# Kernel optimization log

Hardware: AMD Instinct MI355X
Metric: run time of the kernel (lower is better)

Reference implementation:

```python
import jax, jax.numpy as jnp
import numpy as np

B, N, M, H = 32, 1024, 256, 128


def setup_inputs() -> dict:
    key = jax.random.key(0)
    kA, kh, kW1, kW2 = jax.random.split(key, 4)
    A = jax.random.uniform(kA, (B, N, N), dtype=jnp.float32)
    h = jax.random.normal(kh, (B, N, M), dtype=jnp.float32)
    # torch Linear default init scale ~ 1/sqrt(fan_in)
    W1 = jax.random.normal(kW1, (M, H), dtype=jnp.float32) / np.sqrt(M)
    b1 = jnp.zeros((H,), dtype=jnp.float32)
    W2 = jax.random.normal(kW2, (H, M), dtype=jnp.float32) / np.sqrt(H)
    b2 = jnp.zeros((M,), dtype=jnp.float32)
    return {"A": A, "h": h, "W1": W1, "b1": b1, "W2": W2, "b2": b2}


def reference(A, h, W1, b1, W2, b2):
    # k = bmm(A, h) / 3 : [B,N,M]
    k = jnp.einsum('bij,bjm->bim', A, h) / 3.0
    # eta_g: Linear -> ReLU -> Linear
    k = jax.nn.relu(k @ W1 + b1) @ W2 + b2
    # A_mask = max over last dim of A, keepdims -> [B,N,1]
    A_mask = jnp.max(A, axis=-1, keepdims=True)
    # gated combine: k*mask + h*(mask-1)*(-1) == k*mask + h*(1-mask)
    return k * A_mask + h * (1.0 - A_mask)
```

## Files before the change

kernel.cpp:

```cpp
#include <hip/hip_runtime.h>

typedef __attribute__((ext_vector_type(8))) short bf16x8;
typedef __attribute__((ext_vector_type(4))) float f32x4;
typedef __attribute__((ext_vector_type(8))) unsigned short u16x8;

#define BB 32
#define NN 1024
#define MM 256
#define HH 128

__device__ __forceinline__ unsigned short f2bf(float f) {
  union { float f; unsigned int u; } c; c.f = f;
  unsigned int u = c.u + 0x7fffu + ((c.u >> 16) & 1u);
  return (unsigned short)(u >> 16);
}
__device__ __forceinline__ unsigned int cvtpk(float lo, float hi) {
  unsigned int r;
  asm("v_cvt_pk_bf16_f32 %0, %1, %2" : "=v"(r) : "v"(lo), "v"(hi));
  return r;
}
__device__ __forceinline__ float4 gload_f4(const float* p) {
  float4 r;
  asm volatile("global_load_dwordx4 %0, %1, off" : "=v"(r) : "v"(p));
  return r;
}
typedef __attribute__((address_space(3))) unsigned int as3_u32;
typedef const __attribute__((address_space(1))) unsigned int as1_u32;
__device__ __forceinline__ void gl_lds16(const void* g, void* l) {
  __builtin_amdgcn_global_load_lds((as1_u32*)g, (as3_u32*)l, 16, 0, 0);
}

__global__ __launch_bounds__(256)
void k_prep(const float* __restrict__ hg, unsigned short* __restrict__ hTg,
            const float* __restrict__ W1, const float* __restrict__ W2,
            unsigned short* __restrict__ W1T, unsigned short* __restrict__ W2T) {
  int bid = blockIdx.x;
  if (bid < BB * 64) {
    __shared__ unsigned short tile[64][65];
    int b = bid >> 6;
    int t = bid & 63;
    int k0 = (t >> 2) << 6;
    int m0 = (t & 3) << 6;
    int tt = threadIdx.x;
    {
      int r = tt >> 2;
      int cg = (tt & 3) << 4;
      const float* src = hg + (((size_t)b * NN + k0 + r) * MM + m0 + cg);
#pragma unroll
      for (int i = 0; i < 4; ++i) {
        float4 v = reinterpret_cast<const float4*>(src)[i];
        tile[r][cg + i * 4 + 0] = f2bf(v.x);
        tile[r][cg + i * 4 + 1] = f2bf(v.y);
        tile[r][cg + i * 4 + 2] = f2bf(v.z);
        tile[r][cg + i * 4 + 3] = f2bf(v.w);
      }
    }
    __syncthreads();
    {
      int mr = tt >> 2;
      int kc = (tt & 3) << 4;
      alignas(16) unsigned short tmp[16];
#pragma unroll
      for (int i = 0; i < 16; ++i) tmp[i] = tile[kc + i][mr];
      unsigned short* dst = hTg + (((size_t)b * MM + m0 + mr) * NN + k0 + kc);
      *reinterpret_cast<u16x8*>(dst)     = *reinterpret_cast<u16x8*>(tmp);
      *reinterpret_cast<u16x8*>(dst + 8) = *reinterpret_cast<u16x8*>(tmp + 8);
    }
  } else {
    int idx = (bid - BB * 64) * 256 + threadIdx.x;
    if (idx < MM * HH) {
      int hc = idx >> 8;
      int m  = idx & 255;
      W1T[idx] = f2bf(W1[m * HH + hc]);
    } else {
      int j = idx - MM * HH;
      int m  = j >> 7;
      int hd = j & 127;
      W2T[j] = f2bf(W2[hd * MM + m]);
    }
  }
}

#define HB0 0
#define HB1 32768
#define AB0 65536
#define AB1 73728
#define KLD 0
#define CLD 32768
#define SMAXOFF 65536

#define PIPE_BARRIER() do { \
  asm volatile("s_waitcnt lgkmcnt(0)" ::: "memory"); \
  __builtin_amdgcn_s_barrier(); \
  asm volatile("" ::: "memory"); } while (0)

#define VMW(N) do { asm volatile("s_waitcnt vmcnt(" #N ")" ::: "memory"); \
  __builtin_amdgcn_sched_barrier(0); } while (0)

__global__ __launch_bounds__(512)
void k_fused(const float* __restrict__ Ag, const float* __restrict__ hg,
             const unsigned short* __restrict__ hTg,
             const unsigned short* __restrict__ W1Tg,
             const unsigned short* __restrict__ W2Tg,
             const float* __restrict__ b1g, const float* __restrict__ b2g,
             float* __restrict__ outg) {
  __shared__ __align__(16) char smem[81920];
  float* smax = reinterpret_cast<float*>(smem + SMAXOFF);

  const int tid  = threadIdx.x;
  const int lane = tid & 63;
  const int wid  = tid >> 6;
  const int wr   = wid >> 2;
  const int wc   = wid & 3;
  const int l15  = lane & 15;
  const int lg   = lane >> 4;

  const int bid = blockIdx.x;
  const int b   = bid & 31;
  const int r0  = (bid >> 5) << 6;

  const float* Ab = Ag + ((size_t)b * NN + r0) * NN;
  const unsigned short* hTb = hTg + (size_t)b * MM * NN;

  const int arow0 = tid >> 4;
  const int akc   = tid & 15;
  const float* apA0 = Ab + (size_t)arow0        * NN + (akc << 2);
  const float* apA1 = Ab + (size_t)(32 + arow0) * NN + (akc << 2);

  const unsigned short* baseH[4];
#pragma unroll
  for (int i = 0; i < 4; ++i) {
    int c = i * 512 + tid;
    int col = c >> 3, cic = c & 7;
    baseH[i] = hTb + (size_t)col * NN + ((cic ^ (col & 7)) << 3);
  }
  const int ldsW = wid << 10;

#define STAGE_H(K0, HB)                                                     \
  do {                                                                      \
    _Pragma("unroll")                                                       \
    for (int i = 0; i < 4; ++i)                                             \
      gl_lds16(baseH[i] + (K0), smem + (HB) + ldsW + i * 8192);             \
  } while (0)

  float4 rAX0, rAX1, rAY0, rAY1;
#define ISSUE_AX(K0) do { rAX0 = gload_f4(apA0 + (K0));                     \
                          rAX1 = gload_f4(apA1 + (K0)); } while (0)
#define ISSUE_AY(K0) do { rAY0 = gload_f4(apA0 + (K0));                     \
                          rAY1 = gload_f4(apA1 + (K0)); } while (0)

  float pm0 = -1e30f, pm1 = -1e30f;
#define CVTWR(AB, R0, R1)                                                   \
  do {                                                                      \
    pm0 = fmaxf(pm0, fmaxf(fmaxf((R0).x, (R0).y), fmaxf((R0).z, (R0).w)));  \
    pm1 = fmaxf(pm1, fmaxf(fmaxf((R1).x, (R1).y), fmaxf((R1).z, (R1).w)));  \
    uint2 q0 = make_uint2(cvtpk((R0).x, (R0).y), cvtpk((R0).z, (R0).w));    \
    uint2 q1 = make_uint2(cvtpk((R1).x, (R1).y), cvtpk((R1).z, (R1).w));    \
    *reinterpret_cast<uint2*>(smem + (AB) + (arow0)      * 128 +            \
                              ((akc << 3) ^ ((arow0 & 7) << 4))) = q0;      \
    *reinterpret_cast<uint2*>(smem + (AB) + (32 + arow0) * 128 +            \
                              ((akc << 3) ^ ((arow0 & 7) << 4))) = q1;      \
  } while (0)

  f32x4 acc[2][4];
#pragma unroll
  for (int m = 0; m < 2; ++m)
#pragma unroll
    for (int n = 0; n < 4; ++n) acc[m][n] = f32x4{0.f, 0.f, 0.f, 0.f};

#define CONSUME(AB, HB)                                                     \
  do {                                                                      \
    _Pragma("unroll")                                                       \
    for (int kk = 0; kk < 2; ++kk) {                                        \
      const int kb = (kk * 32 + (lg << 3)) * 2;                             \
      bf16x8 af[2], bh[4];                                                  \
      _Pragma("unroll")                                                     \
      for (int m = 0; m < 2; ++m) {                                         \
        int row = (wr << 5) + (m << 4) + l15;                               \
        af[m] = *reinterpret_cast<const bf16x8*>(                           \
            smem + (AB) + row * 128 + (kb ^ ((row & 7) << 4)));             \
      }                                                                     \
      _Pragma("unroll")                                                     \
      for (int n = 0; n < 4; ++n) {                                         \
        int col = (wc << 6) + (n << 4) + l15;                               \
        bh[n] = *reinterpret_cast<const bf16x8*>(                           \
            smem + (HB) + col * 128 + (kb ^ ((col & 7) << 4)));             \
      }                                                                     \
      _Pragma("unroll")                                                     \
      for (int m = 0; m < 2; ++m)                                           \
        _Pragma("unroll")                                                   \
        for (int n = 0; n < 4; ++n)                                         \
          acc[m][n] = __builtin_amdgcn_mfma_f32_16x16x32_bf16(af[m], bh[n], \
                                                              acc[m][n], 0, 0, 0); \
    }                                                                       \
  } while (0)

  STAGE_H(0, HB0);
  ISSUE_AX(0);
  VMW(0);
  CVTWR(AB0, rAX0, rAX1);
  ISSUE_AY(64);
  PIPE_BARRIER();

#pragma unroll
  for (int t = 0; t < 16; ++t) {
    if (t < 15) STAGE_H((t + 1) * 64, (t & 1) ? HB0 : HB1);
    if (t < 14) {
      if (t & 1) ISSUE_AY((t + 2) * 64);
      else       ISSUE_AX((t + 2) * 64);
    }
    CONSUME((t & 1) ? AB1 : AB0, (t & 1) ? HB1 : HB0);
    if (t < 15) {
      if (t < 14) VMW(6); else VMW(4);
      if (t & 1) CVTWR(AB0, rAX0, rAX1);
      else       CVTWR(AB1, rAY0, rAY1);
      if (t < 14) VMW(2); else VMW(0);
      PIPE_BARRIER();
    }
  }

  {
    float v0 = pm0, v1 = pm1;
#pragma unroll
    for (int s = 1; s < 16; s <<= 1) {
      v0 = fmaxf(v0, __shfl_xor(v0, s));
      v1 = fmaxf(v1, __shfl_xor(v1, s));
    }
    if ((tid & 15) == 0) {
      smax[arow0]      = v0;
      smax[32 + arow0] = v1;
    }
  }
  __syncthreads();

  {
    const float inv3 = 1.0f / 3.0f;
#pragma unroll
    for (int m = 0; m < 2; ++m)
#pragma unroll
      for (int n = 0; n < 4; ++n) {
        int col = (wc << 6) + (n << 4) + l15;
#pragma unroll
        for (int j = 0; j < 4; ++j) {
          int row = (wr << 5) + (m << 4) + (lg << 2) + j;
          *reinterpret_cast<unsigned short*>(smem + KLD + row * 512 +
                                             ((col * 2) ^ ((row & 7) << 4))) =
              f2bf(acc[m][n][j] * inv3);
        }
      }
  }
  __syncthreads();

  f32x4 acc1[2][2];
#pragma unroll
  for (int m = 0; m < 2; ++m)
#pragma unroll
    for (int n = 0; n < 2; ++n) acc1[m][n] = f32x4{0.f, 0.f, 0.f, 0.f};
  const int wcol1 = wc << 5;
#pragma unroll
  for (int kq = 0; kq < 8; ++kq) {
    bf16x8 af[2], bw[2];
#pragma unroll
    for (int m = 0; m < 2; ++m) {
      int row = (wr << 5) + (m << 4) + l15;
      af[m] = *reinterpret_cast<const bf16x8*>(smem + KLD + row * 512 +
              (((kq * 32 + (lg << 3)) * 2) ^ ((row & 7) << 4)));
    }
#pragma unroll
    for (int n = 0; n < 2; ++n) {
      int col = wcol1 + (n << 4) + l15;
      bw[n] = *reinterpret_cast<const bf16x8*>(W1Tg + (size_t)col * 256 +
                                               kq * 32 + (lg << 3));
    }
#pragma unroll
    for (int m = 0; m < 2; ++m)
#pragma unroll
      for (int n = 0; n < 2; ++n)
        acc1[m][n] = __builtin_amdgcn_mfma_f32_16x16x32_bf16(af[m], bw[n], acc1[m][n], 0, 0, 0);
  }
  __syncthreads();

  {
#pragma unroll
    for (int n = 0; n < 2; ++n) {
      int col = wcol1 + (n << 4) + l15;
      float bias = b1g[col];
#pragma unroll
      for (int m = 0; m < 2; ++m)
#pragma unroll
        for (int j = 0; j < 4; ++j) {
          int row = (wr << 5) + (m << 4) + (lg << 2) + j;
          float v = fmaxf(acc1[m][n][j] + bias, 0.f);
          *reinterpret_cast<unsigned short*>(smem + CLD + row * 256 +
                                             ((col * 2) ^ ((row & 7) << 4))) = f2bf(v);
        }
    }
  }
  __syncthreads();

  f32x4 acc2[2][4];
#pragma unroll
  for (int m = 0; m < 2; ++m)
#pragma unroll
    for (int n = 0; n < 4; ++n) acc2[m][n] = f32x4{0.f, 0.f, 0.f, 0.f};
#pragma unroll
  for (int kq = 0; kq < 4; ++kq) {
    bf16x8 af[2], bw[4];
#pragma unroll
    for (int m = 0; m < 2; ++m) {
      int row = (wr << 5) + (m << 4) + l15;
      af[m] = *reinterpret_cast<const bf16x8*>(smem + CLD + row * 256 +
              (((kq * 32 + (lg << 3)) * 2) ^ ((row & 7) << 4)));
    }
#pragma unroll
    for (int n = 0; n < 4; ++n) {
      int col = (wc << 6) + (n << 4) + l15;
      bw[n] = *reinterpret_cast<const bf16x8*>(W2Tg + (size_t)col * 128 +
                                               kq * 32 + (lg << 3));
    }
#pragma unroll
    for (int m = 0; m < 2; ++m)
#pragma unroll
      for (int n = 0; n < 4; ++n)
        acc2[m][n] = __builtin_amdgcn_mfma_f32_16x16x32_bf16(af[m], bw[n], acc2[m][n], 0, 0, 0);
  }

  {
#pragma unroll
    for (int n = 0; n < 4; ++n) {
      int col = (wc << 6) + (n << 4) + l15;
      float b2v = b2g[col];
#pragma unroll
      for (int m = 0; m < 2; ++m)
#pragma unroll
        for (int j = 0; j < 4; ++j) {
          int row = (wr << 5) + (m << 4) + (lg << 2) + j;
          float kv = acc2[m][n][j] + b2v;
          float mask = smax[row];
          size_t gidx = ((size_t)b * NN + r0 + row) * MM + col;
          float hv = hg[gidx];
          outg[gidx] = kv * mask + hv * (1.f - mask);
        }
    }
  }
#undef CONSUME
#undef CVTWR
#undef ISSUE_AX
#undef ISSUE_AY
#undef STAGE_H
}

extern "C" void kernel_launch(void* const* d_in, const int* in_sizes, int n_in,
                              void* d_out, int out_size, void* d_ws, size_t ws_size,
                              hipStream_t stream) {
  (void)in_sizes; (void)n_in; (void)out_size; (void)ws_size;
  const float* A  = (const float*)d_in[0];
  const float* h  = (const float*)d_in[1];
  const float* W1 = (const float*)d_in[2];
  const float* b1 = (const float*)d_in[3];
  const float* W2 = (const float*)d_in[4];
  const float* b2 = (const float*)d_in[5];
  float* out = (float*)d_out;

  unsigned short* hT  = (unsigned short*)d_ws;
  unsigned short* W1T = (unsigned short*)((char*)d_ws + (size_t)BB * MM * NN * 2);
  unsigned short* W2T = W1T + MM * HH;

  k_prep<<<BB * 64 + 256, 256, 0, stream>>>(h, hT, W1, W2, W1T, W2T);
  k_fused<<<BB * 16, 512, 0, stream>>>(A, h, hT, W1T, W2T, b1, b2, out);
}
```

Before: 57.94 us.

## Halve K-tile to 32 and shrink shared memory to 40KB

Cuts the K step of the bmm main loop from 64 to 32, doubling the iteration count to 32. Each thread now loads one float4 of A per stage instead of two, and h staging uses two async copies instead of four, with swizzles adjusted for 64-byte rows. Shared memory drops from 80KB to 40KB, presumably to allow more resident blocks or waves per CU. In exchange the kernel takes twice as many barriers and waitcnt syncs, and each sync hides less memory latency. The epilogue buffers now alias at offset 0 (KLD and CLD).

```diff
diff --git a/kernel.cpp b/kernel.cpp
--- a/kernel.cpp
+++ b/kernel.cpp
@@ -82,12 +82,12 @@
 }
 
 #define HB0 0
-#define HB1 32768
-#define AB0 65536
-#define AB1 73728
+#define HB1 16384
+#define AB0 32768
+#define AB1 36864
 #define KLD 0
-#define CLD 32768
-#define SMAXOFF 65536
+#define CLD 0
+#define SMAXOFF 32768
 
 #define PIPE_BARRIER() do { \
   asm volatile("s_waitcnt lgkmcnt(0)" ::: "memory"); \
@@ -104,7 +104,7 @@
              const unsigned short* __restrict__ W2Tg,
              const float* __restrict__ b1g, const float* __restrict__ b2g,
              float* __restrict__ outg) {
-  __shared__ __align__(16) char smem[81920];
+  __shared__ __align__(16) char smem[40960];
   float* smax = reinterpret_cast<float*>(smem + SMAXOFF);
 
   const int tid  = threadIdx.x;
@@ -122,44 +122,36 @@
   const float* Ab = Ag + ((size_t)b * NN + r0) * NN;
   const unsigned short* hTb = hTg + (size_t)b * MM * NN;
 
-  const int arow0 = tid >> 4;
-  const int akc   = tid & 15;
-  const float* apA0 = Ab + (size_t)arow0        * NN + (akc << 2);
-  const float* apA1 = Ab + (size_t)(32 + arow0) * NN + (akc << 2);
-
-  const unsigned short* baseH[4];
-#pragma unroll
-  for (int i = 0; i < 4; ++i) {
+  const int arow = tid >> 3;
+  const int aq   = tid & 7;
+  const float* apA = Ab + (size_t)arow * NN + (aq << 2);
+  const int awb = arow * 64 + (((aq << 3)) ^ ((arow & 3) << 4));
+
+  const unsigned short* baseH[2];
+#pragma unroll
+  for (int i = 0; i < 2; ++i) {
     int c = i * 512 + tid;
-    int col = c >> 3, cic = c & 7;
-    baseH[i] = hTb + (size_t)col * NN + ((cic ^ (col & 7)) << 3);
-  }
-  const int ldsW = wid << 10;
+    int col = c >> 2, sl = c & 3;
+    baseH[i] = hTb + (size_t)col * NN + ((sl ^ (col & 3)) << 3);
+  }
+  const int dstW = wid << 10;
 
 #define STAGE_H(K0, HB)                                                     \
   do {                                                                      \
-    _Pragma("unroll")                                                       \
-    for (int i = 0; i < 4; ++i)                                             \
-      gl_lds16(baseH[i] + (K0), smem + (HB) + ldsW + i * 8192);             \
+    gl_lds16(baseH[0] + (K0), smem + (HB) + dstW);                          \
+    gl_lds16(baseH[1] + (K0), smem + (HB) + 8192 + dstW);                   \
   } while (0)
 
-  float4 rAX0, rAX1, rAY0, rAY1;
-#define ISSUE_AX(K0) do { rAX0 = gload_f4(apA0 + (K0));                     \
-                          rAX1 = gload_f4(apA1 + (K0)); } while (0)
-#define ISSUE_AY(K0) do { rAY0 = gload_f4(apA0 + (K0));                     \
-                          rAY1 = gload_f4(apA1 + (K0)); } while (0)
-
-  float pm0 = -1e30f, pm1 = -1e30f;
-#define CVTWR(AB, R0, R1)                                                   \
+  float4 rAX, rAY;
+#define ISSUE_AX(K0) do { rAX = gload_f4(apA + (K0)); } while (0)
+#define ISSUE_AY(K0) do { rAY = gload_f4(apA + (K0)); } while (0)
+
+  float pmax = -1e30f;
+#define CVTWR(AB, R)                                                        \
   do {                                                                      \
-    pm0 = fmaxf(pm0, fmaxf(fmaxf((R0).x, (R0).y), fmaxf((R0).z, (R0).w)));  \
-    pm1 = fmaxf(pm1, fmaxf(fmaxf((R1).x, (R1).y), fmaxf((R1).z, (R1).w)));  \
-    uint2 q0 = make_uint2(cvtpk((R0).x, (R0).y), cvtpk((R0).z, (R0).w));    \
-    uint2 q1 = make_uint2(cvtpk((R1).x, (R1).y), cvtpk((R1).z, (R1).w));    \
-    *reinterpret_cast<uint2*>(smem + (AB) + (arow0)      * 128 +            \
-                              ((akc << 3) ^ ((arow0 & 7) << 4))) = q0;      \
-    *reinterpret_cast<uint2*>(smem + (AB) + (32 + arow0) * 128 +            \
-                              ((akc << 3) ^ ((arow0 & 7) << 4))) = q1;      \
+    pmax = fmaxf(pmax, fmaxf(fmaxf((R).x, (R).y), fmaxf((R).z, (R).w)));    \
+    uint2 q = make_uint2(cvtpk((R).x, (R).y), cvtpk((R).z, (R).w));         \
+    *reinterpret_cast<uint2*>(smem + (AB) + awb) = q;                       \
   } while (0)
 
   f32x4 acc[2][4];
@@ -170,66 +162,57 @@
 
 #define CONSUME(AB, HB)                                                     \
   do {                                                                      \
+    bf16x8 af[2], bh[4];                                                    \
     _Pragma("unroll")                                                       \
-    for (int kk = 0; kk < 2; ++kk) {                                        \
-      const int kb = (kk * 32 + (lg << 3)) * 2;                             \
-      bf16x8 af[2], bh[4];                                                  \
+    for (int m = 0; m < 2; ++m) {                                           \
+      int row = (wr << 5) + (m << 4) + l15;                                 \
+      af[m] = *reinterpret_cast<const bf16x8*>(                             \
+          smem + (AB) + row * 64 + ((lg << 4) ^ ((row & 3) << 4)));         \
+    }                                                                       \
+    _Pragma("unroll")                                                       \
+    for (int n = 0; n < 4; ++n) {                                           \
+      int col = (wc << 6) + (n << 4) + l15;                                 \
+      bh[n] = *reinterpret_cast<const bf16x8*>(                             \
+          smem + (HB) + col * 64 + ((lg << 4) ^ ((col & 3) << 4)));         \
+    }                                                                       \
+    _Pragma("unroll")                                                       \
+    for (int m = 0; m < 2; ++m)                                             \
       _Pragma("unroll")                                                     \
-      for (int m = 0; m < 2; ++m) {                                         \
-        int row = (wr << 5) + (m << 4) + l15;                               \
-        af[m] = *reinterpret_cast<const bf16x8*>(                           \
-            smem + (AB) + row * 128 + (kb ^ ((row & 7) << 4)));             \
-      }                                                                     \
-      _Pragma("unroll")                                                     \
-      for (int n = 0; n < 4; ++n) {                                         \
-        int col = (wc << 6) + (n << 4) + l15;                               \
-        bh[n] = *reinterpret_cast<const bf16x8*>(                           \
-            smem + (HB) + col * 128 + (kb ^ ((col & 7) << 4)));             \
-      }                                                                     \
-      _Pragma("unroll")                                                     \
-      for (int m = 0; m < 2; ++m)                                           \
-        _Pragma("unroll")                                                   \
-        for (int n = 0; n < 4; ++n)                                         \
-          acc[m][n] = __builtin_amdgcn_mfma_f32_16x16x32_bf16(af[m], bh[n], \
-                                                              acc[m][n], 0, 0, 0); \
-    }                                                                       \
+      for (int n = 0; n < 4; ++n)                                           \
+        acc[m][n] = __builtin_amdgcn_mfma_f32_16x16x32_bf16(af[m], bh[n],   \
+                                                            acc[m][n], 0, 0, 0); \
   } while (0)
 
   STAGE_H(0, HB0);
   ISSUE_AX(0);
   VMW(0);
-  CVTWR(AB0, rAX0, rAX1);
-  ISSUE_AY(64);
+  CVTWR(AB0, rAX);
+  ISSUE_AY(32);
   PIPE_BARRIER();
 
 #pragma unroll
-  for (int t = 0; t < 16; ++t) {
-    if (t < 15) STAGE_H((t + 1) * 64, (t & 1) ? HB0 : HB1);
-    if (t < 14) {
-      if (t & 1) ISSUE_AY((t + 2) * 64);
-      else       ISSUE_AX((t + 2) * 64);
+  for (int t = 0; t < 32; ++t) {
+    if (t < 31) STAGE_H((t + 1) * 32, (t & 1) ? HB0 : HB1);
+    if (t < 30) {
+      if (t & 1) ISSUE_AY((t + 2) * 32);
+      else       ISSUE_AX((t + 2) * 32);
     }
     CONSUME((t & 1) ? AB1 : AB0, (t & 1) ? HB1 : HB0);
-    if (t < 15) {
-      if (t < 14) VMW(6); else VMW(4);
-      if (t & 1) CVTWR(AB0, rAX0, rAX1);
-      else       CVTWR(AB1, rAY0, rAY1);
-      if (t < 14) VMW(2); else VMW(0);
+    if (t < 31) {
+      if (t < 30) VMW(3); else VMW(2);
+      if (t & 1) CVTWR(AB0, rAX);
+      else       CVTWR(AB1, rAY);
+      if (t < 30) VMW(1); else VMW(0);
       PIPE_BARRIER();
     }
   }
 
   {
-    float v0 = pm0, v1 = pm1;
-#pragma unroll
-    for (int s = 1; s < 16; s <<= 1) {
-      v0 = fmaxf(v0, __shfl_xor(v0, s));
-      v1 = fmaxf(v1, __shfl_xor(v1, s));
-    }
-    if ((tid & 15) == 0) {
-      smax[arow0]      = v0;
-      smax[32 + arow0] = v1;
-    }
+    float v = pmax;
+    v = fmaxf(v, __shfl_xor(v, 1));
+    v = fmaxf(v, __shfl_xor(v, 2));
+    v = fmaxf(v, __shfl_xor(v, 4));
+    if ((tid & 7) == 0) smax[arow] = v;
   }
   __syncthreads();
 
```

Measured after the change: 60.95 us. +5.2%, slower.
